# Kernel tuning notes

Hardware: AMD Instinct MI355X
Metric: run time of the kernel (lower is better)

The kernel has to match this reference:

```python
import jax, jax.numpy as jnp
import numpy as np

PLAYERS = 8
DMODEL = 256          # cfg.dmodel (per-embedding dim)
DK = 1024             # cfg.dk
WINDOW = 4096         # cfg.window == T here
A_SPACE = 64
DFULL = DMODEL * 2 * PLAYERS   # 4096, the concatenated model dim


def _positional_encoding(T, dmodel):
    # i = 1/10000^(2j/dmodel); pe[:, ::2]=sin(pos*i), pe[:, 1::2]=cos(pos*i)
    i = 1.0 / jnp.power(jnp.float32(10000.0), jnp.arange(0, dmodel, 2, dtype=jnp.float32) / dmodel)
    pos = jnp.arange(T, dtype=jnp.float32)[:, None]
    pe = jnp.zeros((T, dmodel), dtype=jnp.float32)
    pe = pe.at[:, ::2].set(jnp.sin(pos * i))
    pe = pe.at[:, 1::2].set(jnp.cos(pos * i))
    return pe


def setup_inputs() -> dict:
    key = jax.random.key(0)
    ks = jax.random.split(key, 12)
    n_rows = WINDOW * 2 * PLAYERS  # 65536 one-hot rows
    idx = jax.random.randint(ks[0], (n_rows,), 0, PLAYERS + 1)
    obs = jax.nn.one_hot(idx, PLAYERS + 1, dtype=jnp.int32)
    std = 2.0 / (5.0 * DFULL)  # torch.normal(0, var) uses var as std in the source
    return {
        "obs": obs,
        "o_emb": jax.random.normal(ks[1], (PLAYERS + 1, DMODEL), jnp.float32),
        "d_emb": jax.random.normal(ks[2], (PLAYERS + 1, DMODEL), jnp.float32),
        "WQ": jax.random.normal(ks[3], (DFULL, DK), jnp.float32) * std,
        "WK": jax.random.normal(ks[4], (DFULL, DK), jnp.float32) * std,
        "WV": jax.random.normal(ks[5], (DFULL, DK), jnp.float32) * std,
        "WO": jax.random.normal(ks[6], (DK, DK), jnp.float32) * std,
        "Wo_pol": jax.random.normal(ks[7], (A_SPACE, DK), jnp.float32) * 0.02,
        "bo_pol": jnp.zeros((A_SPACE,), jnp.float32),
        "Wd_pol": jax.random.normal(ks[8], (A_SPACE, DK), jnp.float32) * 0.02,
        "bd_pol": jnp.zeros((A_SPACE,), jnp.float32),
        "Wv": jax.random.normal(ks[9], (1, DK), jnp.float32) * 0.02,
        "bv": jnp.zeros((1,), jnp.float32),
    }


def reference(obs, o_emb, d_emb, WQ, WK, WV, WO, Wo_pol, bo_pol, Wd_pol, bd_pol, Wv, bv):
    obs2 = obs.reshape(-1, PLAYERS + 1)
    # torch.where(row == 1)[1] on one-hot rows == argmax
    idx_o = jnp.argmax(obs2[::2], axis=1)   # [T*players]
    idx_d = jnp.argmax(obs2[1::2], axis=1)  # [T*players]
    emb = jnp.concatenate([o_emb[idx_o], d_emb[idx_d]], axis=1)  # [T*players, 2*dmodel]
    x = emb.reshape(-1, DFULL) * jnp.sqrt(jnp.float32(DMODEL))    # [T, DFULL]
    T = x.shape[0]
    x = x + _positional_encoding(T, DFULL)
    q = x @ WQ  # [T, DK]
    k = x @ WK
    v = x @ WV
    att = jax.nn.softmax((q @ k.T) / jnp.sqrt(jnp.float32(DK)), axis=-1)  # [T, T]
    o = (att @ v) @ WO  # [T, DK]
    h = jax.nn.relu(o[-1])  # last position only, [DK]
    o_logits = h @ Wo_pol.T + bo_pol  # [A_SPACE]
    d_logits = h @ Wd_pol.T + bd_pol  # [A_SPACE]
    value = h @ Wv.T + bv             # [1]
    return (o_logits, d_logits, value)
```

## Files before the change

### kernel.cpp

```cpp
#include <hip/hip_runtime.h>
#include <stdint.h>

#define DK      1024
#define NBLK    256
#define NT      1024
#define LOG2_10000 13.287712379549449f

static const size_t SARR_OFF = 0;
static const size_t KQ_OFF   = 16384;
static const size_t Q_OFF    = 32768;
static const size_t CTX_OFF  = 36864;
static const size_t OL_OFF   = 40960;
static const size_t AXPE_OFF = 45056;
static const size_t W8_OFF   = 61440;
static const size_t MB_OFF   = 66560;

__device__ __forceinline__ unsigned fenc(float x) {
    unsigned u = __float_as_uint(x);
    return (u & 0x80000000u) ? ~u : (u | 0x80000000u);
}
__device__ __forceinline__ float fdec(unsigned e) {
    return (e & 0x80000000u) ? __uint_as_float(e & 0x7FFFFFFFu)
                             : __uint_as_float(~e);
}

__device__ __forceinline__ void stg(float* p, float v) {
    __hip_atomic_store(p, v, __ATOMIC_RELAXED, __HIP_MEMORY_SCOPE_AGENT);
}
__device__ __forceinline__ void stgu(unsigned* p, unsigned v) {
    __hip_atomic_store(p, v, __ATOMIC_RELAXED, __HIP_MEMORY_SCOPE_AGENT);
}
__device__ __forceinline__ float lda(const float* p) {
    return __hip_atomic_load(p, __ATOMIC_RELAXED, __HIP_MEMORY_SCOPE_AGENT);
}
__device__ __forceinline__ unsigned ldau(const unsigned* p) {
    return __hip_atomic_load(p, __ATOMIC_RELAXED, __HIP_MEMORY_SCOPE_AGENT);
}

__device__ unsigned bar_gc[256];
__device__ unsigned bar_gf[256];
__device__ unsigned bar_m[64];

__device__ __forceinline__ unsigned gbar_arrive(int bid) {
    unsigned fl = 0;
    asm volatile("s_waitcnt vmcnt(0)" ::: "memory");
    __syncthreads();
    if (threadIdx.x == 0) {
        unsigned g = (unsigned)bid & 7u;
        unsigned* gc = &bar_gc[g * 32];
        unsigned* gf = &bar_gf[g * 32];
        fl = __hip_atomic_load(gf, __ATOMIC_RELAXED, __HIP_MEMORY_SCOPE_AGENT);
        unsigned old = __hip_atomic_fetch_add(gc, 1u, __ATOMIC_RELAXED,
                                              __HIP_MEMORY_SCOPE_AGENT);
        if (old == 31u) {
            __hip_atomic_store(gc, 0u, __ATOMIC_RELAXED,
                               __HIP_MEMORY_SCOPE_AGENT);
            unsigned gen = __hip_atomic_load(&bar_m[32], __ATOMIC_RELAXED,
                                             __HIP_MEMORY_SCOPE_AGENT);
            unsigned o2 = __hip_atomic_fetch_add(&bar_m[0], 1u, __ATOMIC_RELAXED,
                                                 __HIP_MEMORY_SCOPE_AGENT);
            if (o2 == 7u) {
                __hip_atomic_store(&bar_m[0], 0u, __ATOMIC_RELAXED,
                                   __HIP_MEMORY_SCOPE_AGENT);
                __hip_atomic_store(&bar_m[32], gen + 1u, __ATOMIC_RELEASE,
                                   __HIP_MEMORY_SCOPE_AGENT);
            } else {
                int gd = 0;
                while (__hip_atomic_load(&bar_m[32], __ATOMIC_RELAXED,
                                         __HIP_MEMORY_SCOPE_AGENT) == gen) {
                    __builtin_amdgcn_s_sleep(1);
                    if (++gd > (1 << 16)) break;
                }
            }
            __hip_atomic_store(gf, fl + 1u, __ATOMIC_RELEASE,
                               __HIP_MEMORY_SCOPE_AGENT);
        }
    }
    return fl;
}

__device__ __forceinline__ void gbar_wait(int bid, unsigned fl) {
    if (threadIdx.x == 0) {
        unsigned g = (unsigned)bid & 7u;
        unsigned* gf = &bar_gf[g * 32];
        int gd = 0;
        while (__hip_atomic_load(gf, __ATOMIC_RELAXED,
                                 __HIP_MEMORY_SCOPE_AGENT) == fl) {
            __builtin_amdgcn_s_sleep(1);
            if (++gd > (1 << 16)) break;
        }
    }
    __syncthreads();
}

__device__ __forceinline__ void gbar(int bid) { gbar_wait(bid, gbar_arrive(bid)); }

__device__ __forceinline__ float4 bred4(float4 a, float* buf, int tid) {
    #pragma unroll
    for (int off = 32; off; off >>= 1) {
        a.x += __shfl_down(a.x, off, 64);
        a.y += __shfl_down(a.y, off, 64);
        a.z += __shfl_down(a.z, off, 64);
        a.w += __shfl_down(a.w, off, 64);
    }
    float4* b4 = (float4*)buf;
    if ((tid & 63) == 0) b4[tid >> 6] = a;
    __syncthreads();
    float4 r = {0.f, 0.f, 0.f, 0.f};
    if (tid == 0) {
        #pragma unroll
        for (int i = 0; i < 16; ++i) {
            float4 t = b4[i];
            r.x += t.x; r.y += t.y; r.z += t.z; r.w += t.w;
        }
    }
    __syncthreads();
    return r;
}

__global__ __launch_bounds__(1024, 4) void fused_k(
        const int*   __restrict__ obs,
        const float* __restrict__ o_emb,  const float* __restrict__ d_emb,
        const float* __restrict__ WQ,     const float* __restrict__ WK,
        const float* __restrict__ WV,     const float* __restrict__ WO,
        const float* __restrict__ Wo_pol, const float* __restrict__ bo_pol,
        const float* __restrict__ Wd_pol, const float* __restrict__ bd_pol,
        const float* __restrict__ Wv,     const float* __restrict__ bv,
        float* __restrict__ out,          char* __restrict__ ws) {

    float* sarr = (float*)(ws + SARR_OFF);
    float* kq   = (float*)(ws + KQ_OFF);
    float* qg   = (float*)(ws + Q_OFF);
    float* ctx  = (float*)(ws + CTX_OFF);
    float* ol   = (float*)(ws + OL_OFF);
    float* axpe = (float*)(ws + AXPE_OFF);
    float* w8   = (float*)(ws + W8_OFF);
    unsigned* mbits = (unsigned*)(ws + MB_OFF);

    __shared__ __align__(16) float smem[12288];
    unsigned char* sidx = (unsigned char*)&smem[12224];

    int bid = blockIdx.x, tid = threadIdx.x;
    const int w = ((bid & 7) << 5) | (bid >> 3);

    {
        float* lx   = smem;
        int*   lidx = (int*)&smem[4096];
        if (tid < 256) {
            int g = w * 256 + tid;
            const int* r = obs + (size_t)g * 9;
            int id = 0;
            #pragma unroll
            for (int j = 1; j < 9; ++j) id += j * r[j];
            sidx[(tid & ~15) | ((tid & 1) << 3) | ((tid >> 1) & 7)] =
                (unsigned char)id;
        }
        if (tid < 16) {
            const int* rr = obs + (size_t)(65520 + tid) * 9;
            int id2 = 0;
            #pragma unroll
            for (int j = 1; j < 9; ++j) id2 += j * rr[j];
            lidx[(tid & 1) * 8 + (tid >> 1)] = id2;
        }
        if (w == 255) {
            for (int i = tid; i < 1281; i += NT) {
                if (i < 1280) stg(&w8[i], 0.0f);
                else          stgu(mbits, 0u);
            }
        }
        __syncthreads();
        #pragma unroll
        for (int i = 0; i < 4; ++i) {
            int c = tid + NT * i;
            int p = c >> 9, rr2 = c & 511;
            int seg, r2; const float* tab;
            if (rr2 < 256) { seg = p;     r2 = rr2;       tab = o_emb; }
            else           { seg = 8 + p; r2 = rr2 - 256; tab = d_emb; }
            float e = tab[lidx[seg] * 256 + r2];
            float f = exp2f(-((float)(c & ~1) * (1.0f / 4096.0f)) * LOG2_10000);
            float sv, cv;
            __sincosf(4095.0f * f, &sv, &cv);
            lx[c] = e * 16.0f + ((c & 1) ? cv : sv);
        }
        __syncthreads();
        const float4* W4 = (const float4*)WQ;
        float4 acc = {0.f, 0.f, 0.f, 0.f};
        #pragma unroll
        for (int i = 0; i < 4; ++i) {
            int k = tid + NT * i;
            float xv = lx[k];
            float4 wv = W4[(size_t)k * 256 + w];
            acc.x += xv * wv.x; acc.y += xv * wv.y;
            acc.z += xv * wv.z; acc.w += xv * wv.w;
        }
        float4 s4 = bred4(acc, &smem[4112], tid);
        if (tid == 0) {
            stg(&qg[w * 4 + 0], s4.x); stg(&qg[w * 4 + 1], s4.y);
            stg(&qg[w * 4 + 2], s4.z); stg(&qg[w * 4 + 3], s4.w);
        }
    }
    gbar(bid);

    {
        float* qls = smem;
        qls[tid] = lda(&qg[tid]);
        __syncthreads();
        int wv_ = tid >> 6, lane = tid & 63;
        int cc = w * 16 + wv_;
        const float4* W4 = (const float4*)(WK + (size_t)cc * DK);
        const float4* q4 = (const float4*)qls;
        float acc = 0.0f;
        #pragma unroll
        for (int i = 0; i < 4; ++i) {
            float4 wvv = W4[i * 64 + lane];
            float4 qq  = q4[i * 64 + lane];
            acc += wvv.x * qq.x + wvv.y * qq.y + wvv.z * qq.z + wvv.w * qq.w;
        }
        #pragma unroll
        for (int off = 32; off; off >>= 1) acc += __shfl_down(acc, off, 64);
        if (lane == 0) stg(&kq[cc], acc * (1.0f / 32.0f));
    }
    {
        unsigned fl = gbar_arrive(bid);
        float* lemb = &smem[4096];
        float* lfrq = &smem[8724];
        for (int i = tid; i < 2048; i += NT)
            lfrq[i] = exp2f(-((float)(2 * i) * (1.0f / 4096.0f)) * LOG2_10000);
        for (int i = tid; i < 4608; i += NT) {
            int row = i >> 8, r = i & 255;
            lemb[row * 257 + r] = (row < 9) ? o_emb[row * 256 + r]
                                            : d_emb[(row - 9) * 256 + r];
        }
        gbar_wait(bid, fl);
    }

    {
        float* lkq   = smem;
        float* lemb  = &smem[4096];
        float* lfrq  = &smem[8724];
        float* ldot4 = &smem[10772];
        float* lped  = &smem[11348];
        #pragma unroll
        for (int i = 0; i < 4; ++i) {
            int c = tid + NT * i;
            lkq[c] = lda(&kq[c]);
        }
        __syncthreads();
        if (tid < 576) {
            int p = tid >> 2, q = tid & 3;
            int sg = p / 9, id = p % 9;
            int base = (sg < 8) ? sg * 512 : (sg - 8) * 512 + 256;
            const float* e = lemb + ((sg < 8) ? id : (9 + id)) * 257;
            float a = 0.0f;
            for (int i = 0; i < 64; ++i) {
                int r = q * 64 + ((i + q * 13) & 63);
                a += e[r] * lkq[base + r];
            }
            ldot4[tid] = a;
        }
        int tt = tid >> 6, sub = tid & 63;
        int t = w * 16 + tt;
        float acc = 0.0f;
        #pragma unroll 4
        for (int jj = 0; jj < 32; ++jj) {
            int jf = jj * 64 + sub;
            float f = lfrq[jf];
            float svv, cvv;
            __sincosf((float)t * f, &svv, &cvv);
            acc += svv * lkq[2 * jf] + cvv * lkq[2 * jf + 1];
        }
        #pragma unroll
        for (int off = 32; off; off >>= 1) acc += __shfl_down(acc, off, 64);
        if (sub == 0) lped[tt] = acc;
        __syncthreads();
        if (tid < 16) {
            int t2 = w * 16 + tid;
            float tot = lped[tid];
            const uint32_t* ip = (const uint32_t*)(sidx + tid * 16);
            uint32_t u0 = ip[0], u1 = ip[1], u2 = ip[2], u3 = ip[3];
            #pragma unroll
            for (int sg = 0; sg < 16; ++sg) {
                uint32_t u = (sg < 4) ? u0 : (sg < 8) ? u1 : (sg < 12) ? u2 : u3;
                int id = (u >> ((sg & 3) * 8)) & 0xFF;
                int p = (sg * 9 + id) * 4;
                tot += 16.0f * (ldot4[p] + ldot4[p + 1] + ldot4[p + 2] + ldot4[p + 3]);
            }
            stg(&sarr[t2], tot);
            atomicMax(mbits, fenc(tot));
        }
    }
    gbar(bid);

    {
        float* le  = smem;
        float* pss = &smem[4352];
        float* psc = &smem[5376];
        float* lh  = &smem[6400];
        float m = fdec(ldau(mbits));
        if (tid < 144) lh[tid] = 0.0f;
        #pragma unroll
        for (int i = 0; i < 4; ++i) {
            int c = tid + NT * i;
            le[c] = expf(lda(&sarr[c]) - m);
        }
        __syncthreads();
        if (tid < 256) {
            int lt = tid >> 4, seg = tid & 15;
            int id = sidx[lt * 16 + seg];
            atomicAdd(&lh[seg * 9 + id], le[w * 16 + lt]);
        }
        int jl = tid >> 7, tseg = tid & 127;
        int j = w * 8 + jl;
        float f = exp2f(-((float)(2 * j) * (1.0f / 4096.0f)) * LOG2_10000);
        float sf, cf;
        __sincosf(f, &sf, &cf);
        int t0 = tseg * 32;
        float sv, cv;
        __sincosf((float)t0 * f, &sv, &cv);
        float ss = 0.f, sc = 0.f;
        #pragma unroll
        for (int i = 0; i < 32; ++i) {
            float a = le[t0 + i];
            ss += a * sv; sc += a * cv;
            float ns = sv * cf + cv * sf;
            cv = cv * cf - sv * sf;
            sv = ns;
        }
        pss[tid] = ss; psc[tid] = sc;
        __syncthreads();
        if (tid < 144) atomicAdd(&w8[(bid & 7) * 160 + tid], lh[tid]);
        if (tid < 512) {
            int m2 = tid >> 6, l = tid & 63;
            float a  = pss[m2 * 128 + l] + pss[m2 * 128 + 64 + l];
            float b2 = psc[m2 * 128 + l] + psc[m2 * 128 + 64 + l];
            #pragma unroll
            for (int off = 32; off; off >>= 1) {
                a  += __shfl_down(a, off, 64);
                b2 += __shfl_down(b2, off, 64);
            }
            if (l == 0) {
                int jj = w * 8 + m2;
                stg(&axpe[2 * jj],     a);
                stg(&axpe[2 * jj + 1], b2);
            }
        }
    }
    {
        unsigned fl = gbar_arrive(bid);
        float* lembE = &smem[7168];
        for (int i = tid; i < 4608; i += NT) {
            int row = i >> 8, r = i & 255;
            lembE[row * 257 + r] = (row < 9) ? o_emb[row * 256 + r]
                                             : d_emb[(row - 9) * 256 + r];
        }
        gbar_wait(bid, fl);
    }

    {
        float* lw    = smem;
        float* lembE = &smem[7168];
        if (tid < 144) {
            float tsum = 0.0f;
            #pragma unroll
            for (int g2 = 0; g2 < 8; ++g2) tsum += lda(&w8[g2 * 160 + tid]);
            lw[tid] = tsum;
        }
        __syncthreads();
        if (tid == 0) {
            float z = 0.0f;
            #pragma unroll
            for (int i = 0; i < 144; ++i) z += lw[i];
            smem[144] = 16.0f / z;
        }
        __syncthreads();
        const float4* WV4 = (const float4*)WV;
        float4 acc = {0.f, 0.f, 0.f, 0.f};
        #pragma unroll
        for (int i = 0; i < 4; ++i) {
            int c = tid + NT * i;
            int p = c >> 9, rr = c & 511;
            int seg = (rr < 256) ? p : 8 + p;
            int r   = (rr < 256) ? rr : rr - 256;
            int rbase = (rr < 256) ? 0 : 9;
            float a = 0.0f;
            #pragma unroll
            for (int id2 = 0; id2 < 9; ++id2)
                a += lw[seg * 9 + id2] * lembE[(rbase + id2) * 257 + r];
            float ax = lda(&axpe[c]) + 16.0f * a;
            float4 wv = WV4[(size_t)c * 256 + w];
            acc.x += ax * wv.x; acc.y += ax * wv.y;
            acc.z += ax * wv.z; acc.w += ax * wv.w;
        }
        float4 s4 = bred4(acc, &smem[160], tid);
        if (tid == 0) {
            float iz = smem[144];
            stg(&ctx[w * 4 + 0], s4.x * iz); stg(&ctx[w * 4 + 1], s4.y * iz);
            stg(&ctx[w * 4 + 2], s4.z * iz); stg(&ctx[w * 4 + 3], s4.w * iz);
        }
    }
    gbar(bid);

    {
        float* lc = smem;
        lc[tid] = lda(&ctx[tid]);
        __syncthreads();
        const float4* WO4 = (const float4*)WO;
        float cj = lc[tid];
        float4 wvv = WO4[(size_t)tid * 256 + w];
        float4 acc = {cj * wvv.x, cj * wvv.y, cj * wvv.z, cj * wvv.w};
        float4 s4 = bred4(acc, &smem[1024], tid);
        if (tid == 0) {
            stg(&ol[w * 4 + 0], s4.x); stg(&ol[w * 4 + 1], s4.y);
            stg(&ol[w * 4 + 2], s4.z); stg(&ol[w * 4 + 3], s4.w);
        }
    }
    {
        unsigned fl = gbar_arrive(bid);
        float wvh = 0.0f, bh = 0.0f;
        if (w < 129) {
            const float* Wh;
            if (w < 64)       { Wh = Wo_pol + (size_t)w * DK;        bh = bo_pol[w]; }
            else if (w < 128) { Wh = Wd_pol + (size_t)(w - 64) * DK; bh = bd_pol[w - 64]; }
            else              { Wh = Wv;                              bh = bv[0]; }
            wvh = Wh[tid];
        }
        gbar_wait(bid, fl);

        if (w < 129) {
            float sacc = fmaxf(lda(&ol[tid]), 0.0f) * wvh;
            #pragma unroll
            for (int off = 32; off; off >>= 1) sacc += __shfl_down(sacc, off, 64);
            float* red = smem;
            if ((tid & 63) == 0) red[tid >> 6] = sacc;
            __syncthreads();
            if (tid == 0) {
                float tot = bh;
                #pragma unroll
                for (int i = 0; i < 16; ++i) tot += red[i];
                out[w] = tot;
            }
        }
    }
}

extern "C" void kernel_launch(void* const* d_in, const int* in_sizes, int n_in,
                              void* d_out, int out_size, void* d_ws, size_t ws_size,
                              hipStream_t stream) {
    const int*   obs    = (const int*)  d_in[0];
    const float* o_emb  = (const float*)d_in[1];
    const float* d_emb  = (const float*)d_in[2];
    const float* WQ     = (const float*)d_in[3];
    const float* WK     = (const float*)d_in[4];
    const float* WV     = (const float*)d_in[5];
    const float* WO     = (const float*)d_in[6];
    const float* Wo_pol = (const float*)d_in[7];
    const float* bo_pol = (const float*)d_in[8];
    const float* Wd_pol = (const float*)d_in[9];
    const float* bd_pol = (const float*)d_in[10];
    const float* Wv     = (const float*)d_in[11];
    const float* bv     = (const float*)d_in[12];
    float* out = (float*)d_out;
    char* ws   = (char*)d_ws;

    fused_k<<<dim3(NBLK), dim3(NT), 0, stream>>>(
        obs, o_emb, d_emb, WQ, WK, WV, WO,
        Wo_pol, bo_pol, Wd_pol, bd_pol, Wv, bv, out, ws);
}
```

Measured before the change: 157.9 us.

## Split-K partial sums with atomics and double-buffered scratch to cut grid barriers

```diff
diff --git a/kernel.cpp b/kernel.cpp
--- a/kernel.cpp
+++ b/kernel.cpp
@@ -6,40 +6,23 @@
 #define NT      1024
 #define LOG2_10000 13.287712379549449f
 
-static const size_t SARR_OFF = 0;
-static const size_t KQ_OFF   = 16384;
-static const size_t Q_OFF    = 32768;
-static const size_t CTX_OFF  = 36864;
-static const size_t OL_OFF   = 40960;
-static const size_t AXPE_OFF = 45056;
-static const size_t W8_OFF   = 61440;
-static const size_t MB_OFF   = 66560;
-
-__device__ __forceinline__ unsigned fenc(float x) {
-    unsigned u = __float_as_uint(x);
-    return (u & 0x80000000u) ? ~u : (u | 0x80000000u);
-}
-__device__ __forceinline__ float fdec(unsigned e) {
-    return (e & 0x80000000u) ? __uint_as_float(e & 0x7FFFFFFFu)
-                             : __uint_as_float(~e);
-}
-
-__device__ __forceinline__ void stg(float* p, float v) {
-    __hip_atomic_store(p, v, __ATOMIC_RELAXED, __HIP_MEMORY_SCOPE_AGENT);
-}
-__device__ __forceinline__ void stgu(unsigned* p, unsigned v) {
-    __hip_atomic_store(p, v, __ATOMIC_RELAXED, __HIP_MEMORY_SCOPE_AGENT);
-}
-__device__ __forceinline__ float lda(const float* p) {
-    return __hip_atomic_load(p, __ATOMIC_RELAXED, __HIP_MEMORY_SCOPE_AGENT);
-}
-__device__ __forceinline__ unsigned ldau(const unsigned* p) {
-    return __hip_atomic_load(p, __ATOMIC_RELAXED, __HIP_MEMORY_SCOPE_AGENT);
-}
+__device__ float g_sarr[4096];
+__device__ float g_kq[4096];
+__device__ float g_ol[1024];
+__device__ float g_q8[2][8][1024];
+__device__ float g_ctx8[2][8][1024];
+__device__ float g_w8[2][8][160];
 
 __device__ unsigned bar_gc[256];
 __device__ unsigned bar_gf[256];
 __device__ unsigned bar_m[64];
+
+__device__ __forceinline__ void stg(float* p, float v) {
+    __hip_atomic_store(p, v, __ATOMIC_RELAXED, __HIP_MEMORY_SCOPE_AGENT);
+}
+__device__ __forceinline__ float lda(const float* p) {
+    return __hip_atomic_load(p, __ATOMIC_RELAXED, __HIP_MEMORY_SCOPE_AGENT);
+}
 
 __device__ __forceinline__ unsigned gbar_arrive(int bid) {
     unsigned fl = 0;
@@ -127,25 +110,35 @@
         const float* __restrict__ Wd_pol, const float* __restrict__ bd_pol,
         const float* __restrict__ Wv,     const float* __restrict__ bv,
         float* __restrict__ out,          char* __restrict__ ws) {
-
-    float* sarr = (float*)(ws + SARR_OFF);
-    float* kq   = (float*)(ws + KQ_OFF);
-    float* qg   = (float*)(ws + Q_OFF);
-    float* ctx  = (float*)(ws + CTX_OFF);
-    float* ol   = (float*)(ws + OL_OFF);
-    float* axpe = (float*)(ws + AXPE_OFF);
-    float* w8   = (float*)(ws + W8_OFF);
-    unsigned* mbits = (unsigned*)(ws + MB_OFF);
-
-    __shared__ __align__(16) float smem[12288];
-    unsigned char* sidx = (unsigned char*)&smem[12224];
+    (void)ws;
+
+    __shared__ __align__(16) float smem[12416];
+    float* axpeL = &smem[12288];
+    unsigned char* sidx = (unsigned char*)&smem[12304];
 
     int bid = blockIdx.x, tid = threadIdx.x;
-    const int w = ((bid & 7) << 5) | (bid >> 3);
-
-    {
-        float* lx   = smem;
-        int*   lidx = (int*)&smem[4096];
+    const int w  = ((bid & 7) << 5) | (bid >> 3);
+    const int sh = bid & 7;
+
+    const unsigned genv = __hip_atomic_load(&bar_m[32], __ATOMIC_RELAXED,
+                                            __HIP_MEMORY_SCOPE_AGENT);
+    const int par = (int)((genv / 6u) & 1u);
+    float* q8  = &g_q8[par][0][0];
+    float* q8n = &g_q8[par ^ 1][0][0];
+    float* c8  = &g_ctx8[par][0][0];
+    float* c8n = &g_ctx8[par ^ 1][0][0];
+    float* w8  = &g_w8[par][0][0];
+    float* w8n = &g_w8[par ^ 1][0][0];
+
+    {
+        if (tid < 69) {
+            int idx = w * 69 + tid;
+            if (idx < 8192)       stg(&q8n[idx], 0.0f);
+            else if (idx < 16384) stg(&c8n[idx - 8192], 0.0f);
+            else                  stg(&w8n[idx - 16384], 0.0f);
+        }
+        int* lidx = (int*)&smem[4100];
+        float* lx = &smem[4120];
         if (tid < 256) {
             int g = w * 256 + tid;
             const int* r = obs + (size_t)g * 9;
@@ -162,63 +155,43 @@
             for (int j = 1; j < 9; ++j) id2 += j * rr[j];
             lidx[(tid & 1) * 8 + (tid >> 1)] = id2;
         }
-        if (w == 255) {
-            for (int i = tid; i < 1281; i += NT) {
-                if (i < 1280) stg(&w8[i], 0.0f);
-                else          stgu(mbits, 0u);
-            }
-        }
-        __syncthreads();
-        #pragma unroll
-        for (int i = 0; i < 4; ++i) {
-            int c = tid + NT * i;
-            int p = c >> 9, rr2 = c & 511;
-            int seg, r2; const float* tab;
-            if (rr2 < 256) { seg = p;     r2 = rr2;       tab = o_emb; }
-            else           { seg = 8 + p; r2 = rr2 - 256; tab = d_emb; }
-            float e = tab[lidx[seg] * 256 + r2];
+        __syncthreads();
+        if (tid < 16) {
+            int c = w * 16 + tid;
+            int p = c >> 9, rr = c & 511;
+            const float* tab = (rr < 256) ? o_emb : d_emb;
+            int slot = (rr < 256) ? p : 8 + p;
+            int r2 = rr & 255;
+            float e = tab[lidx[slot] * 256 + r2];
             float f = exp2f(-((float)(c & ~1) * (1.0f / 4096.0f)) * LOG2_10000);
             float sv, cv;
             __sincosf(4095.0f * f, &sv, &cv);
-            lx[c] = e * 16.0f + ((c & 1) ? cv : sv);
-        }
-        __syncthreads();
+            lx[tid] = e * 16.0f + ((c & 1) ? cv : sv);
+        }
+        __syncthreads();
+        int ksub = tid >> 8, n4 = tid & 255;
         const float4* W4 = (const float4*)WQ;
         float4 acc = {0.f, 0.f, 0.f, 0.f};
         #pragma unroll
-        for (int i = 0; i < 4; ++i) {
-            int k = tid + NT * i;
+        for (int kk = 0; kk < 4; ++kk) {
+            int k = ksub * 4 + kk;
             float xv = lx[k];
-            float4 wv = W4[(size_t)k * 256 + w];
+            float4 wv = W4[(size_t)(w * 16 + k) * 256 + n4];
             acc.x += xv * wv.x; acc.y += xv * wv.y;
             acc.z += xv * wv.z; acc.w += xv * wv.w;
         }
-        float4 s4 = bred4(acc, &smem[4112], tid);
-        if (tid == 0) {
-            stg(&qg[w * 4 + 0], s4.x); stg(&qg[w * 4 + 1], s4.y);
-            stg(&qg[w * 4 + 2], s4.z); stg(&qg[w * 4 + 3], s4.w);
-        }
-    }
-    gbar(bid);
-
-    {
-        float* qls = smem;
-        qls[tid] = lda(&qg[tid]);
-        __syncthreads();
-        int wv_ = tid >> 6, lane = tid & 63;
-        int cc = w * 16 + wv_;
-        const float4* W4 = (const float4*)(WK + (size_t)cc * DK);
-        const float4* q4 = (const float4*)qls;
-        float acc = 0.0f;
-        #pragma unroll
-        for (int i = 0; i < 4; ++i) {
-            float4 wvv = W4[i * 64 + lane];
-            float4 qq  = q4[i * 64 + lane];
-            acc += wvv.x * qq.x + wvv.y * qq.y + wvv.z * qq.z + wvv.w * qq.w;
-        }
-        #pragma unroll
-        for (int off = 32; off; off >>= 1) acc += __shfl_down(acc, off, 64);
-        if (lane == 0) stg(&kq[cc], acc * (1.0f / 32.0f));
+        float4* p4 = (float4*)smem;
+        p4[ksub * 256 + n4] = acc;
+        __syncthreads();
+        if (tid < 256) {
+            float4 a = p4[tid], b = p4[256 + tid],
+                   c2 = p4[512 + tid], d = p4[768 + tid];
+            float* dst = &q8[sh * 1024 + tid * 4];
+            atomicAdd(dst + 0, a.x + b.x + c2.x + d.x);
+            atomicAdd(dst + 1, a.y + b.y + c2.y + d.y);
+            atomicAdd(dst + 2, a.z + b.z + c2.z + d.z);
+            atomicAdd(dst + 3, a.w + b.w + c2.w + d.w);
+        }
     }
     {
         unsigned fl = gbar_arrive(bid);
@@ -235,6 +208,30 @@
     }
 
     {
+        float* qsum = &smem[10772];
+        float t = 0.0f;
+        #pragma unroll
+        for (int s2 = 0; s2 < 8; ++s2) t += lda(&q8[s2 * 1024 + tid]);
+        qsum[tid] = t;
+        __syncthreads();
+        int wv_ = tid >> 6, lane = tid & 63;
+        int cc = w * 16 + wv_;
+        const float4* W4 = (const float4*)(WK + (size_t)cc * DK);
+        const float4* q4 = (const float4*)qsum;
+        float acc = 0.0f;
+        #pragma unroll
+        for (int i = 0; i < 4; ++i) {
+            float4 wvv = W4[i * 64 + lane];
+            float4 qq  = q4[i * 64 + lane];
+            acc += wvv.x * qq.x + wvv.y * qq.y + wvv.z * qq.z + wvv.w * qq.w;
+        }
+        #pragma unroll
+        for (int off = 32; off; off >>= 1) acc += __shfl_down(acc, off, 64);
+        if (lane == 0) stg(&g_kq[cc], acc * (1.0f / 32.0f));
+    }
+    gbar(bid);
+
+    {
         float* lkq   = smem;
         float* lemb  = &smem[4096];
         float* lfrq  = &smem[8724];
@@ -243,7 +240,7 @@
         #pragma unroll
         for (int i = 0; i < 4; ++i) {
             int c = tid + NT * i;
-            lkq[c] = lda(&kq[c]);
+            lkq[c] = lda(&g_kq[c]);
         }
         __syncthreads();
         if (tid < 576) {
@@ -285,36 +282,47 @@
                 int p = (sg * 9 + id) * 4;
                 tot += 16.0f * (ldot4[p] + ldot4[p + 1] + ldot4[p + 2] + ldot4[p + 3]);
             }
-            stg(&sarr[t2], tot);
-            atomicMax(mbits, fenc(tot));
+            stg(&g_sarr[t2], tot);
         }
     }
     gbar(bid);
 
     {
-        float* le  = smem;
-        float* pss = &smem[4352];
-        float* psc = &smem[5376];
-        float* lh  = &smem[6400];
-        float m = fdec(ldau(mbits));
+        float* le   = smem;
+        float* pss  = &smem[4352];
+        float* psc  = &smem[5376];
+        float* lh   = &smem[6400];
+        float* mred = &smem[6560];
+        float sv4[4];
+        float mx = -3.4e38f;
+        #pragma unroll
+        for (int i = 0; i < 4; ++i) {
+            float v = lda(&g_sarr[tid + NT * i]);
+            sv4[i] = v;
+            mx = fmaxf(mx, v);
+        }
+        #pragma unroll
+        for (int off = 32; off; off >>= 1) mx = fmaxf(mx, __shfl_down(mx, off, 64));
+        if ((tid & 63) == 0) mred[tid >> 6] = mx;
+        __syncthreads();
+        float m = mred[0];
+        #pragma unroll
+        for (int i = 1; i < 16; ++i) m = fmaxf(m, mred[i]);
+        #pragma unroll
+        for (int i = 0; i < 4; ++i) le[tid + NT * i] = expf(sv4[i] - m);
         if (tid < 144) lh[tid] = 0.0f;
-        #pragma unroll
-        for (int i = 0; i < 4; ++i) {
-            int c = tid + NT * i;
-            le[c] = expf(lda(&sarr[c]) - m);
-        }
         __syncthreads();
         if (tid < 256) {
             int lt = tid >> 4, seg = tid & 15;
             int id = sidx[lt * 16 + seg];
             atomicAdd(&lh[seg * 9 + id], le[w * 16 + lt]);
         }
-        int jl = tid >> 7, tseg = tid & 127;
+        int jl = tid >> 7, ts = tid & 127;
         int j = w * 8 + jl;
         float f = exp2f(-((float)(2 * j) * (1.0f / 4096.0f)) * LOG2_10000);
         float sf, cf;
         __sincosf(f, &sf, &cf);
-        int t0 = tseg * 32;
+        int t0 = ts * 32;
         float sv, cv;
         __sincosf((float)t0 * f, &sv, &cv);
         float ss = 0.f, sc = 0.f;
@@ -328,7 +336,7 @@
         }
         pss[tid] = ss; psc[tid] = sc;
         __syncthreads();
-        if (tid < 144) atomicAdd(&w8[(bid & 7) * 160 + tid], lh[tid]);
+        if (tid < 144) atomicAdd(&w8[sh * 160 + tid], lh[tid]);
         if (tid < 512) {
             int m2 = tid >> 6, l = tid & 63;
             float a  = pss[m2 * 128 + l] + pss[m2 * 128 + 64 + l];
@@ -338,80 +346,82 @@
                 a  += __shfl_down(a, off, 64);
                 b2 += __shfl_down(b2, off, 64);
             }
-            if (l == 0) {
-                int jj = w * 8 + m2;
-                stg(&axpe[2 * jj],     a);
-                stg(&axpe[2 * jj + 1], b2);
-            }
-        }
-    }
-    {
-        unsigned fl = gbar_arrive(bid);
-        float* lembE = &smem[7168];
-        for (int i = tid; i < 4608; i += NT) {
-            int row = i >> 8, r = i & 255;
-            lembE[row * 257 + r] = (row < 9) ? o_emb[row * 256 + r]
-                                             : d_emb[(row - 9) * 256 + r];
-        }
-        gbar_wait(bid, fl);
-    }
-
-    {
-        float* lw    = smem;
-        float* lembE = &smem[7168];
+            if (l == 0) { axpeL[2 * m2] = a; axpeL[2 * m2 + 1] = b2; }
+        }
+    }
+    gbar(bid);
+
+    {
+        float* lw  = &smem[4352];
+        float* axv = &smem[4512];
         if (tid < 144) {
-            float tsum = 0.0f;
-            #pragma unroll
-            for (int g2 = 0; g2 < 8; ++g2) tsum += lda(&w8[g2 * 160 + tid]);
-            lw[tid] = tsum;
+            float t = 0.0f;
+            #pragma unroll
+            for (int s2 = 0; s2 < 8; ++s2) t += lda(&w8[s2 * 160 + tid]);
+            lw[tid] = t;
         }
         __syncthreads();
         if (tid == 0) {
             float z = 0.0f;
             #pragma unroll
             for (int i = 0; i < 144; ++i) z += lw[i];
-            smem[144] = 16.0f / z;
-        }
-        __syncthreads();
+            smem[4496] = 16.0f / z;
+        }
+        if (tid < 16) {
+            int c = w * 16 + tid;
+            int p = c >> 9, rr = c & 511;
+            const float* tab = (rr < 256) ? o_emb : d_emb;
+            int slot = (rr < 256) ? p : 8 + p;
+            int r2 = rr & 255;
+            float a = 0.0f;
+            #pragma unroll
+            for (int id2 = 0; id2 < 9; ++id2)
+                a += lw[slot * 9 + id2] * tab[id2 * 256 + r2];
+            axv[tid] = axpeL[tid] + 16.0f * a;
+        }
+        __syncthreads();
+        float iz = smem[4496];
+        int ksub = tid >> 8, n4 = tid & 255;
         const float4* WV4 = (const float4*)WV;
         float4 acc = {0.f, 0.f, 0.f, 0.f};
         #pragma unroll
-        for (int i = 0; i < 4; ++i) {
-            int c = tid + NT * i;
-            int p = c >> 9, rr = c & 511;
-            int seg = (rr < 256) ? p : 8 + p;
-            int r   = (rr < 256) ? rr : rr - 256;
-            int rbase = (rr < 256) ? 0 : 9;
-            float a = 0.0f;
-            #pragma unroll
-            for (int id2 = 0; id2 < 9; ++id2)
-                a += lw[seg * 9 + id2] * lembE[(rbase + id2) * 257 + r];
-            float ax = lda(&axpe[c]) + 16.0f * a;
-            float4 wv = WV4[(size_t)c * 256 + w];
-            acc.x += ax * wv.x; acc.y += ax * wv.y;
-            acc.z += ax * wv.z; acc.w += ax * wv.w;
-        }
-        float4 s4 = bred4(acc, &smem[160], tid);
+        for (int kk = 0; kk < 4; ++kk) {
+            int k = ksub * 4 + kk;
+            float av = axv[k];
+            float4 wv = WV4[(size_t)(w * 16 + k) * 256 + n4];
+            acc.x += av * wv.x; acc.y += av * wv.y;
+            acc.z += av * wv.z; acc.w += av * wv.w;
+        }
+        float4* p4 = (float4*)smem;
+        p4[ksub * 256 + n4] = acc;
+        __syncthreads();
+        if (tid < 256) {
+            float4 a = p4[tid], b = p4[256 + tid],
+                   c2 = p4[512 + tid], d = p4[768 + tid];
+            float* dst = &c8[sh * 1024 + tid * 4];
+            atomicAdd(dst + 0, (a.x + b.x + c2.x + d.x) * iz);
+            atomicAdd(dst + 1, (a.y + b.y + c2.y + d.y) * iz);
+            atomicAdd(dst + 2, (a.z + b.z + c2.z + d.z) * iz);
+            atomicAdd(dst + 3, (a.w + b.w + c2.w + d.w) * iz);
+        }
+    }
+    {
+        unsigned fl = gbar_arrive(bid);
+        float4 wo = ((const float4*)WO)[(size_t)tid * 256 + w];
+        ((float4*)&smem[6144])[tid] = wo;
+        gbar_wait(bid, fl);
+    }
+
+    {
+        float cj = 0.0f;
+        #pragma unroll
+        for (int s2 = 0; s2 < 8; ++s2) cj += lda(&c8[s2 * 1024 + tid]);
+        float4 wo = ((float4*)&smem[6144])[tid];
+        float4 acc = {cj * wo.x, cj * wo.y, cj * wo.z, cj * wo.w};
+        float4 s4 = bred4(acc, &smem[10496], tid);
         if (tid == 0) {
-            float iz = smem[144];
-            stg(&ctx[w * 4 + 0], s4.x * iz); stg(&ctx[w * 4 + 1], s4.y * iz);
-            stg(&ctx[w * 4 + 2], s4.z * iz); stg(&ctx[w * 4 + 3], s4.w * iz);
-        }
-    }
-    gbar(bid);
-
-    {
-        float* lc = smem;
-        lc[tid] = lda(&ctx[tid]);
-        __syncthreads();
-        const float4* WO4 = (const float4*)WO;
-        float cj = lc[tid];
-        float4 wvv = WO4[(size_t)tid * 256 + w];
-        float4 acc = {cj * wvv.x, cj * wvv.y, cj * wvv.z, cj * wvv.w};
-        float4 s4 = bred4(acc, &smem[1024], tid);
-        if (tid == 0) {
-            stg(&ol[w * 4 + 0], s4.x); stg(&ol[w * 4 + 1], s4.y);
-            stg(&ol[w * 4 + 2], s4.z); stg(&ol[w * 4 + 3], s4.w);
+            stg(&g_ol[w * 4 + 0], s4.x); stg(&g_ol[w * 4 + 1], s4.y);
+            stg(&g_ol[w * 4 + 2], s4.z); stg(&g_ol[w * 4 + 3], s4.w);
         }
     }
     {
@@ -427,7 +437,7 @@
         gbar_wait(bid, fl);
 
         if (w < 129) {
-            float sacc = fmaxf(lda(&ol[tid]), 0.0f) * wvh;
+            float sacc = fmaxf(lda(&g_ol[tid]), 0.0f) * wvh;
             #pragma unroll
             for (int off = 32; off; off >>= 1) sacc += __shfl_down(sacc, off, 64);
             float* red = smem;
```

New measurement: 157.0 us. About the same (-0.6%).
